# Kernel optimization log

Hardware: AMD Instinct MI355X
Metric: run time of the kernel (lower is better)

Reference implementation:

```python
import jax, jax.numpy as jnp
import numpy as np

D = 128
NH = 8
L = 3
DFF = 2048
DEPOT_IDX = 0
LN_EPS = 1e-5


def _ln(x, g, b):
    m = jnp.mean(x, -1, keepdims=True)
    v = jnp.mean((x - m) ** 2, -1, keepdims=True)
    return (x - m) / jnp.sqrt(v + LN_EPS) * g + b


def _mha(x, wqkv, bqkv, wo, bo):
    # torch nn.MultiheadAttention, batch_first, no dropout (eval)
    b, n, d = x.shape
    hd = d // NH
    qkv = x @ wqkv.T + bqkv                       # [b,n,3d]
    q, k, v = jnp.split(qkv, 3, axis=-1)
    sh = lambda t: t.reshape(b, n, NH, hd).transpose(0, 2, 1, 3)
    q, k, v = sh(q), sh(k), sh(v)
    att = jax.nn.softmax(jnp.einsum('bhqd,bhkd->bhqk', q, k) * (hd ** -0.5), axis=-1)
    o = jnp.einsum('bhqk,bhkd->bhqd', att, v).transpose(0, 2, 1, 3).reshape(b, n, d)
    return o @ wo.T + bo


def _encoder(c, w_inp, b_inp, wqkv, bqkv, wo, bo, w1, b1, w2, b2, g1, be1, g2, be2):
    h = c @ w_inp.T + b_inp                       # [b,n,d]

    def layer(h, p):
        (wqkv, bqkv, wo, bo, w1, b1, w2, b2, g1, be1, g2, be2) = p
        # post-LN TransformerEncoderLayer (torch default norm_first=False, relu)
        h = _ln(h + _mha(h, wqkv, bqkv, wo, bo), g1, be1)
        ff = jax.nn.relu(h @ w1.T + b1) @ w2.T + b2
        h = _ln(h + ff, g2, be2)
        return h, None

    h, _ = jax.lax.scan(layer, h, (wqkv, bqkv, wo, bo, w1, b1, w2, b2, g1, be1, g2, be2))
    return h


def _greedy(c, start_node, params):
    (w_inp, b_inp, wqkv, bqkv, wo, bo, w1, b1, w2, b2, g1, be1, g2, be2,
     wq, bq, wk, bk) = params
    b, n, _ = c.shape
    e = _encoder(c, w_inp, b_inp, wqkv, bqkv, wo, bo, w1, b1, w2, b2, g1, be1, g2, be2)
    kproj = e @ wk.T + bk                          # [b,n,d], hoisted (loop-invariant)
    scale = D ** (-0.5)
    neg = jnp.finfo(e.dtype).min
    bidx = jnp.arange(b)

    vis0 = jnp.zeros((b, n), bool).at[:, DEPOT_IDX].set(True)

    def step(carry, _):
        node, vis = carry
        mask = vis.at[bidx, node].set(True)
        q = e[bidx, node] @ wq.T + bq              # [b,d]
        logits = jnp.einsum('bd,bnd->bn', q, kproj) * scale
        logits = jnp.where(mask, neg, logits)
        nxt = jnp.argmax(logits, axis=-1)
        return (nxt, mask), (node, logits)

    (_, _), (tour, logits) = jax.lax.scan(step, (start_node, vis0), None, length=n - 1)
    return tour.T, logits.transpose(1, 0, 2)      # [b,n-1], [b,n-1,n]


def setup_inputs() -> dict:
    key = jax.random.key(0)
    ks = jax.random.split(key, 24)
    B, N = 512, 100
    w = lambda k, s: jax.random.normal(k, s, jnp.float32) * 0.05
    inp = {
        'c': jax.random.uniform(ks[0], (B, N, 2), jnp.float32),
        'start_node': jax.random.randint(ks[1], (B,), 1, N),
        'w_inp': w(ks[2], (D, 2)), 'b_inp': jnp.zeros((D,), jnp.float32),
        'wqkv': w(ks[3], (L, 3 * D, D)), 'bqkv': jnp.zeros((L, 3 * D), jnp.float32),
        'wo': w(ks[4], (L, D, D)), 'bo': jnp.zeros((L, D), jnp.float32),
        'w1': w(ks[5], (L, DFF, D)), 'b1': jnp.zeros((L, DFF), jnp.float32),
        'w2': w(ks[6], (L, D, DFF)), 'b2': jnp.zeros((L, D), jnp.float32),
        'g1': jnp.ones((L, D), jnp.float32), 'be1': jnp.zeros((L, D), jnp.float32),
        'g2': jnp.ones((L, D), jnp.float32), 'be2': jnp.zeros((L, D), jnp.float32),
        'wq': w(ks[7], (D, D)), 'bq': jnp.zeros((D,), jnp.float32),
        'wk': w(ks[8], (D, D)), 'bk': jnp.zeros((D,), jnp.float32),
    }
    return inp


def reference(c, start_node, w_inp, b_inp, wqkv, bqkv, wo, bo, w1, b1, w2, b2,
              g1, be1, g2, be2, wq, bq, wk, bk):
    params = (w_inp, b_inp, wqkv, bqkv, wo, bo, w1, b1, w2, b2,
              g1, be1, g2, be2, wq, bq, wk, bk)
    tour, logits = _greedy(c, start_node, params)
    return tour, logits
```

## Files before the change

### kernel.cpp

```cpp
#include <hip/hip_runtime.h>
#include <hip/hip_bf16.h>
#include <math.h>

#define D 128
#define NH 8
#define HD 16
#define NL 3
#define DFF 2048
#define NNODE 100
#define BATCH 512
#define M_TOT (BATCH * NNODE)
#define LN_EPS 1e-5f
#define NEGW (-3.0e+38f)

typedef __attribute__((ext_vector_type(8))) short bf16x8;
typedef __attribute__((ext_vector_type(4))) float f32x4;
typedef __attribute__((ext_vector_type(8))) unsigned short u16x8;

__device__ __forceinline__ unsigned short f2bf(float x) {
  unsigned u = __float_as_uint(x);
  u = u + 0x7FFFu + ((u >> 16) & 1u);
  return (unsigned short)(u >> 16);
}
__device__ __forceinline__ float bf2f(unsigned short s) {
  return __uint_as_float(((unsigned)s) << 16);
}

__global__ __launch_bounds__(256) void k_split(
    const float* __restrict__ src, unsigned short* __restrict__ hi,
    unsigned short* __restrict__ lo, int n) {
  int i = blockIdx.x * 256 + threadIdx.x;
  if (i >= n) return;
  float x = src[i];
  unsigned short h = f2bf(x);
  hi[i] = h;
  lo[i] = f2bf(x - bf2f(h));
}

__global__ __launch_bounds__(256) void k_inproj(
    const float* __restrict__ c, const float* __restrict__ w,
    const float* __restrict__ b, float* __restrict__ h,
    unsigned short* __restrict__ hhi, unsigned short* __restrict__ hlo) {
  int idx = blockIdx.x * 256 + threadIdx.x;
  if (idx >= M_TOT * D) return;
  int m = idx >> 7, d = idx & 127;
  float v = c[m * 2] * w[d * 2] + c[m * 2 + 1] * w[d * 2 + 1] + b[d];
  h[idx] = v;
  unsigned short t = f2bf(v);
  hhi[idx] = t;
  hlo[idx] = f2bf(v - bf2f(t));
}

__global__ __launch_bounds__(256) void k_gemm3(
    const unsigned short* __restrict__ Ah, const unsigned short* __restrict__ Al,
    const unsigned short* __restrict__ Wh, const unsigned short* __restrict__ Wl,
    const float* __restrict__ bias,
    float* __restrict__ C, unsigned short* __restrict__ Chi,
    unsigned short* __restrict__ Clo, int M, int N, int K, int relu_split) {
  __shared__ unsigned short sAh[64 * 40], sAl[64 * 40];
  __shared__ unsigned short sWh[128 * 40], sWl[128 * 40];
  const int m0 = blockIdx.x * 64, n0 = blockIdx.y * 128;
  const int tid = threadIdx.x, lane = tid & 63, wid = tid >> 6;
  const int wr = wid >> 1, wc = wid & 1;
  const int lr = lane & 15, lg = lane >> 4;
  f32x4 acc[2][4];
#pragma unroll
  for (int a = 0; a < 2; ++a)
#pragma unroll
    for (int b = 0; b < 4; ++b) acc[a][b] = (f32x4){0.f, 0.f, 0.f, 0.f};
  const int ar = tid >> 2, ak = (tid & 3) * 8;
  const int wrr = tid >> 1, wkk = (tid & 1) * 16;
  const bool a_ok = (m0 + ar) < M;
  const long long a_base = (long long)(m0 + ar) * K + ak;
  const long long w_base = (long long)(n0 + wrr) * K + wkk;
  for (int k0 = 0; k0 < K; k0 += 32) {
    u16x8 vah = {0, 0, 0, 0, 0, 0, 0, 0}, val = {0, 0, 0, 0, 0, 0, 0, 0};
    if (a_ok) {
      vah = *(const u16x8*)(Ah + a_base + k0);
      val = *(const u16x8*)(Al + a_base + k0);
    }
    u16x8 vwh0 = *(const u16x8*)(Wh + w_base + k0);
    u16x8 vwh1 = *(const u16x8*)(Wh + w_base + k0 + 8);
    u16x8 vwl0 = *(const u16x8*)(Wl + w_base + k0);
    u16x8 vwl1 = *(const u16x8*)(Wl + w_base + k0 + 8);
    __syncthreads();
    *(u16x8*)&sAh[ar * 40 + ak] = vah;
    *(u16x8*)&sAl[ar * 40 + ak] = val;
    *(u16x8*)&sWh[wrr * 40 + wkk] = vwh0;
    *(u16x8*)&sWh[wrr * 40 + wkk + 8] = vwh1;
    *(u16x8*)&sWl[wrr * 40 + wkk] = vwl0;
    *(u16x8*)&sWl[wrr * 40 + wkk + 8] = vwl1;
    __syncthreads();
    bf16x8 fah[2], fal[2], fwh[4], fwl[4];
#pragma unroll
    for (int fm = 0; fm < 2; ++fm) {
      int o = (wr * 32 + fm * 16 + lr) * 40 + lg * 8;
      fah[fm] = *(const bf16x8*)&sAh[o];
      fal[fm] = *(const bf16x8*)&sAl[o];
    }
#pragma unroll
    for (int fn = 0; fn < 4; ++fn) {
      int o = (wc * 64 + fn * 16 + lr) * 40 + lg * 8;
      fwh[fn] = *(const bf16x8*)&sWh[o];
      fwl[fn] = *(const bf16x8*)&sWl[o];
    }
#pragma unroll
    for (int fm = 0; fm < 2; ++fm)
#pragma unroll
      for (int fn = 0; fn < 4; ++fn) {
        acc[fm][fn] = __builtin_amdgcn_mfma_f32_16x16x32_bf16(
            fah[fm], fwl[fn], acc[fm][fn], 0, 0, 0);
        acc[fm][fn] = __builtin_amdgcn_mfma_f32_16x16x32_bf16(
            fal[fm], fwh[fn], acc[fm][fn], 0, 0, 0);
        acc[fm][fn] = __builtin_amdgcn_mfma_f32_16x16x32_bf16(
            fah[fm], fwh[fn], acc[fm][fn], 0, 0, 0);
      }
  }
#pragma unroll
  for (int fm = 0; fm < 2; ++fm) {
    int rb = m0 + wr * 32 + fm * 16 + lg * 4;
#pragma unroll
    for (int fn = 0; fn < 4; ++fn) {
      int col = n0 + wc * 64 + fn * 16 + lr;
      float bv = bias[col];
#pragma unroll
      for (int j = 0; j < 4; ++j) {
        int row = rb + j;
        if (row < M) {
          float v = acc[fm][fn][j] + bv;
          if (relu_split) {
            v = fmaxf(v, 0.f);
            unsigned short hv = f2bf(v);
            long long o = (long long)row * N + col;
            Chi[o] = hv;
            Clo[o] = f2bf(v - bf2f(hv));
          } else {
            C[(long long)row * N + col] = v;
          }
        }
      }
    }
  }
}

__global__ __launch_bounds__(256) void k_gemm3_ln(
    const unsigned short* __restrict__ Ah, const unsigned short* __restrict__ Al,
    const unsigned short* __restrict__ Wh, const unsigned short* __restrict__ Wl,
    const float* __restrict__ bias, const float* __restrict__ g,
    const float* __restrict__ be, float* __restrict__ hres,
    unsigned short* __restrict__ hhi, unsigned short* __restrict__ hlo,
    int M, int K) {
  __shared__ unsigned short sAh[64 * 40], sAl[64 * 40];
  __shared__ unsigned short sWh[128 * 40], sWl[128 * 40];
  __shared__ float redS[64][2];
  __shared__ float redQ[64][2];
  const int m0 = blockIdx.x * 64;
  const int tid = threadIdx.x, lane = tid & 63, wid = tid >> 6;
  const int wr = wid >> 1, wc = wid & 1;
  const int lr = lane & 15, lg = lane >> 4;
  f32x4 acc[2][4];
#pragma unroll
  for (int a = 0; a < 2; ++a)
#pragma unroll
    for (int b = 0; b < 4; ++b) acc[a][b] = (f32x4){0.f, 0.f, 0.f, 0.f};
  const int ar = tid >> 2, ak = (tid & 3) * 8;
  const int wrr = tid >> 1, wkk = (tid & 1) * 16;
  const bool a_ok = (m0 + ar) < M;
  const long long a_base = (long long)(m0 + ar) * K + ak;
  const long long w_base = (long long)wrr * K + wkk;
  for (int k0 = 0; k0 < K; k0 += 32) {
    u16x8 vah = {0, 0, 0, 0, 0, 0, 0, 0}, val = {0, 0, 0, 0, 0, 0, 0, 0};
    if (a_ok) {
      vah = *(const u16x8*)(Ah + a_base + k0);
      val = *(const u16x8*)(Al + a_base + k0);
    }
    u16x8 vwh0 = *(const u16x8*)(Wh + w_base + k0);
    u16x8 vwh1 = *(const u16x8*)(Wh + w_base + k0 + 8);
    u16x8 vwl0 = *(const u16x8*)(Wl + w_base + k0);
    u16x8 vwl1 = *(const u16x8*)(Wl + w_base + k0 + 8);
    __syncthreads();
    *(u16x8*)&sAh[ar * 40 + ak] = vah;
    *(u16x8*)&sAl[ar * 40 + ak] = val;
    *(u16x8*)&sWh[wrr * 40 + wkk] = vwh0;
    *(u16x8*)&sWh[wrr * 40 + wkk + 8] = vwh1;
    *(u16x8*)&sWl[wrr * 40 + wkk] = vwl0;
    *(u16x8*)&sWl[wrr * 40 + wkk + 8] = vwl1;
    __syncthreads();
    bf16x8 fah[2], fal[2], fwh[4], fwl[4];
#pragma unroll
    for (int fm = 0; fm < 2; ++fm) {
      int o = (wr * 32 + fm * 16 + lr) * 40 + lg * 8;
      fah[fm] = *(const bf16x8*)&sAh[o];
      fal[fm] = *(const bf16x8*)&sAl[o];
    }
#pragma unroll
    for (int fn = 0; fn < 4; ++fn) {
      int o = (wc * 64 + fn * 16 + lr) * 40 + lg * 8;
      fwh[fn] = *(const bf16x8*)&sWh[o];
      fwl[fn] = *(const bf16x8*)&sWl[o];
    }
#pragma unroll
    for (int fm = 0; fm < 2; ++fm)
#pragma unroll
      for (int fn = 0; fn < 4; ++fn) {
        acc[fm][fn] = __builtin_amdgcn_mfma_f32_16x16x32_bf16(
            fah[fm], fwl[fn], acc[fm][fn], 0, 0, 0);
        acc[fm][fn] = __builtin_amdgcn_mfma_f32_16x16x32_bf16(
            fal[fm], fwh[fn], acc[fm][fn], 0, 0, 0);
        acc[fm][fn] = __builtin_amdgcn_mfma_f32_16x16x32_bf16(
            fah[fm], fwh[fn], acc[fm][fn], 0, 0, 0);
      }
  }
  float x[2][4][4];
#pragma unroll
  for (int fm = 0; fm < 2; ++fm)
#pragma unroll
    for (int fn = 0; fn < 4; ++fn) {
      int col = wc * 64 + fn * 16 + lr;
      float bv = bias[col];
#pragma unroll
      for (int j = 0; j < 4; ++j) {
        int row = m0 + wr * 32 + fm * 16 + lg * 4 + j;
        float r = (row < M) ? hres[(long long)row * D + col] : 0.f;
        x[fm][fn][j] = acc[fm][fn][j] + bv + r;
      }
    }
#pragma unroll
  for (int fm = 0; fm < 2; ++fm)
#pragma unroll
    for (int j = 0; j < 4; ++j) {
      float s = x[fm][0][j] + x[fm][1][j] + x[fm][2][j] + x[fm][3][j];
      s += __shfl_xor(s, 1);
      s += __shfl_xor(s, 2);
      s += __shfl_xor(s, 4);
      s += __shfl_xor(s, 8);
      if (lr == 0) redS[wr * 32 + fm * 16 + lg * 4 + j][wc] = s;
    }
  __syncthreads();
  float mean[2][4];
#pragma unroll
  for (int fm = 0; fm < 2; ++fm)
#pragma unroll
    for (int j = 0; j < 4; ++j) {
      int rl = wr * 32 + fm * 16 + lg * 4 + j;
      mean[fm][j] = (redS[rl][0] + redS[rl][1]) * (1.f / 128.f);
      float d0 = x[fm][0][j] - mean[fm][j];
      float d1 = x[fm][1][j] - mean[fm][j];
      float d2 = x[fm][2][j] - mean[fm][j];
      float d3 = x[fm][3][j] - mean[fm][j];
      float q = d0 * d0 + d1 * d1 + d2 * d2 + d3 * d3;
      q += __shfl_xor(q, 1);
      q += __shfl_xor(q, 2);
      q += __shfl_xor(q, 4);
      q += __shfl_xor(q, 8);
      if (lr == 0) redQ[rl][wc] = q;
    }
  __syncthreads();
#pragma unroll
  for (int fm = 0; fm < 2; ++fm)
#pragma unroll
    for (int j = 0; j < 4; ++j) {
      int rl = wr * 32 + fm * 16 + lg * 4 + j;
      int row = m0 + rl;
      if (row >= M) continue;
      float var = (redQ[rl][0] + redQ[rl][1]) * (1.f / 128.f);
      float sd = sqrtf(var + LN_EPS);
#pragma unroll
      for (int fn = 0; fn < 4; ++fn) {
        int col = wc * 64 + fn * 16 + lr;
        float o = (x[fm][fn][j] - mean[fm][j]) / sd * g[col] + be[col];
        long long ix = (long long)row * D + col;
        hres[ix] = o;
        unsigned short t = f2bf(o);
        hhi[ix] = t;
        hlo[ix] = f2bf(o - bf2f(t));
      }
    }
}

__global__ __launch_bounds__(256) void k_gemm(
    const float* __restrict__ A, long long sA,
    const float* __restrict__ W, long long sW,
    const float* __restrict__ bias,
    float* __restrict__ C, long long sC,
    int M, int N, int K, float scale, int relu) {
  __shared__ float As[32][72];
  __shared__ float Ws[32][72];
  A += (long long)blockIdx.z * sA;
  W += (long long)blockIdx.z * sW;
  C += (long long)blockIdx.z * sC;
  int m0 = blockIdx.x * 64, n0 = blockIdx.y * 64;
  int tid = threadIdx.x;
  int lx = tid & 31, ly = tid >> 5;
  int tc = tid & 15, tr = tid >> 4;
  float acc[4][4] = {};
  for (int k0 = 0; k0 < K; k0 += 32) {
#pragma unroll
    for (int i = 0; i < 8; ++i) {
      int m = m0 + ly + i * 8;
      As[lx][ly + i * 8] = (m < M) ? A[(long long)m * K + k0 + lx] : 0.f;
      int n = n0 + ly + i * 8;
      Ws[lx][ly + i * 8] = (n < N) ? W[(long long)n * K + k0 + lx] : 0.f;
    }
    __syncthreads();
#pragma unroll
    for (int k = 0; k < 32; ++k) {
      float4 av = *(const float4*)&As[k][tr * 4];
      float4 wv = *(const float4*)&Ws[k][tc * 4];
      const float* ap = (const float*)&av;
      const float* wp = (const float*)&wv;
#pragma unroll
      for (int i = 0; i < 4; ++i)
#pragma unroll
        for (int j = 0; j < 4; ++j)
          acc[i][j] = fmaf(ap[i], wp[j], acc[i][j]);
    }
    __syncthreads();
  }
#pragma unroll
  for (int i = 0; i < 4; ++i) {
    int m = m0 + tr * 4 + i;
    if (m >= M) continue;
#pragma unroll
    for (int j = 0; j < 4; ++j) {
      int n = n0 + tc * 4 + j;
      if (n >= N) continue;
      float v = acc[i][j] * scale;
      if (bias) v += bias[n];
      if (relu) v = fmaxf(v, 0.f);
      C[(long long)m * N + n] = v;
    }
  }
}

__global__ __launch_bounds__(256) void k_attn(
    const float* __restrict__ qkv, unsigned short* __restrict__ aoh,
    unsigned short* __restrict__ aol) {
  __shared__ float Qs[NNODE][20];
  __shared__ float Ks[NNODE][20];
  __shared__ float Vs[NNODE][20];
  __shared__ float Ss[NNODE][101];
  int bh = blockIdx.x;
  int b = bh >> 3, hh = bh & 7;
  const float* base = qkv + (long long)b * NNODE * 384 + hh * HD;
  int tid = threadIdx.x;
  for (int idx = tid; idx < NNODE * HD; idx += 256) {
    int n = idx >> 4, d2 = idx & 15;
    Qs[n][d2] = base[(long long)n * 384 + d2];
    Ks[n][d2] = base[(long long)n * 384 + 128 + d2];
    Vs[n][d2] = base[(long long)n * 384 + 256 + d2];
  }
  __syncthreads();
  for (int p = tid; p < NNODE * NNODE; p += 256) {
    int i = p / 100, j = p - i * 100;
    const float4* qv = (const float4*)&Qs[i][0];
    const float4* kv = (const float4*)&Ks[j][0];
    float s = 0.f;
#pragma unroll
    for (int t = 0; t < 4; ++t) {
      float4 q = qv[t], k = kv[t];
      s = fmaf(q.x, k.x, s);
      s = fmaf(q.y, k.y, s);
      s = fmaf(q.z, k.z, s);
      s = fmaf(q.w, k.w, s);
    }
    Ss[i][j] = s * 0.25f;
  }
  __syncthreads();
  float* red = (float*)Qs;
  int r = tid >> 1, hf = tid & 1;
  float* row = &Ss[r][hf * 50];
  if (tid < 200) {
    float mx = row[0];
    for (int j = 1; j < 50; ++j) mx = fmaxf(mx, row[j]);
    red[tid] = mx;
  }
  __syncthreads();
  if (tid < 200) {
    float mx = fmaxf(red[r * 2], red[r * 2 + 1]);
    float sum = 0.f;
    for (int j = 0; j < 50; ++j) {
      float e = expf(row[j] - mx);
      row[j] = e;
      sum += e;
    }
    red[256 + tid] = sum;
  }
  __syncthreads();
  if (tid < 200) {
    float tot = red[256 + r * 2] + red[256 + r * 2 + 1];
    for (int j = 0; j < 50; ++j) row[j] = row[j] / tot;
  }
  __syncthreads();
  for (int p = tid; p < NNODE * HD; p += 256) {
    int i = p >> 4, d2 = p & 15;
    float o = 0.f;
    for (int k = 0; k < NNODE; ++k) o = fmaf(Ss[i][k], Vs[k][d2], o);
    long long idx = ((long long)b * NNODE + i) * D + hh * HD + d2;
    unsigned short hv = f2bf(o);
    aoh[idx] = hv;
    aol[idx] = f2bf(o - bf2f(hv));
  }
}

__global__ __launch_bounds__(64) void k_decode(
    const float* __restrict__ S, const int* __restrict__ start,
    float* __restrict__ tour, float* __restrict__ logits) {
  __shared__ float Sl[NNODE * NNODE];
  int b = blockIdx.x;
  const float* Sg = S + (long long)b * NNODE * NNODE;
  int l = threadIdx.x;
  for (int i = l; i < NNODE * NNODE; i += 64) Sl[i] = Sg[i];
  __syncthreads();
  unsigned long long visLo = 1ull, visHi = 0ull;
  int node = start[b];
  float* lg = logits + (long long)b * 99 * 100;
  for (int t = 0; t < 99; ++t) {
    if (node < 64) visLo |= 1ull << node;
    else visHi |= 1ull << (node - 64);
    const float* row = &Sl[node * 100];
    float c0 = ((visLo >> l) & 1ull) ? NEGW : row[l];
    float c1 = NEGW;
    int j2 = l + 64;
    if (j2 < NNODE && !((visHi >> l) & 1ull)) c1 = row[j2];
    lg[t * 100 + l] = c0;
    if (j2 < NNODE) lg[t * 100 + j2] = c1;
    if (l == 0) tour[b * 99 + t] = (float)node;
    float v = c0;
    int idx = l;
    if (c1 > v) { v = c1; idx = j2; }
    for (int off = 32; off; off >>= 1) {
      float ov = __shfl_xor(v, off);
      int oi = __shfl_xor(idx, off);
      if (ov > v || (ov == v && oi < idx)) { v = ov; idx = oi; }
    }
    node = idx;
  }
}

extern "C" void kernel_launch(void* const* d_in, const int* in_sizes, int n_in,
                              void* d_out, int out_size, void* d_ws, size_t ws_size,
                              hipStream_t stream) {
  const float* c     = (const float*)d_in[0];
  const int*   start = (const int*)d_in[1];
  const float* w_inp = (const float*)d_in[2];
  const float* b_inp = (const float*)d_in[3];
  const float* wqkv  = (const float*)d_in[4];
  const float* bqkv  = (const float*)d_in[5];
  const float* wo    = (const float*)d_in[6];
  const float* bo    = (const float*)d_in[7];
  const float* w1    = (const float*)d_in[8];
  const float* b1    = (const float*)d_in[9];
  const float* w2    = (const float*)d_in[10];
  const float* b2    = (const float*)d_in[11];
  const float* g1    = (const float*)d_in[12];
  const float* be1   = (const float*)d_in[13];
  const float* g2    = (const float*)d_in[14];
  const float* be2   = (const float*)d_in[15];
  const float* wq    = (const float*)d_in[16];
  const float* bq    = (const float*)d_in[17];
  const float* wk    = (const float*)d_in[18];
  const float* bk    = (const float*)d_in[19];

  float* h = (float*)d_ws;
  unsigned short* h_hi = (unsigned short*)((char*)d_ws + 26214400);
  unsigned short* h_lo = h_hi + (size_t)M_TOT * D;
  unsigned short* wsp  = (unsigned short*)((char*)d_ws + 52428800);
  unsigned short* wqkvh = wsp;
  unsigned short* wqkvl = wsp + 147456;
  unsigned short* woh   = wsp + 294912;
  unsigned short* wol   = wsp + 344064;
  unsigned short* w1h   = wsp + 393216;
  unsigned short* w1l   = wsp + 1179648;
  unsigned short* w2h   = wsp + 1966080;
  unsigned short* w2l   = wsp + 2752512;
  unsigned short* wqh   = wsp + 3538944;
  unsigned short* wql   = wsp + 3555328;
  unsigned short* wkh   = wsp + 3571712;
  unsigned short* wkl   = wsp + 3588096;
  float* wsArena = (float*)((char*)d_ws + 59637760);
  long long R = (long long)ws_size - 59637760LL;
  if (R < 0) R = 0;

  float* tour   = (float*)d_out;
  float* logits = (float*)d_out + (size_t)BATCH * (NNODE - 1);
  long long LBYTES = (long long)BATCH * (NNODE - 1) * NNODE * 4;

  float* encArena = (R >= LBYTES) ? wsArena : logits;
  long long E = (R >= LBYTES) ? R : LBYTES;

  long long CB = E / 204800;
  if (CB < 1) CB = 1;
  if (CB > BATCH) CB = BATCH;
  long long RB = (E / 8192) & ~3LL;
  if (RB < 4) RB = 4;
  if (RB > M_TOT) RB = M_TOT;
  long long CB2 = R / 142400;
  if (CB2 < 1) CB2 = 1;
  if (CB2 > BATCH) CB2 = BATCH;

  k_split<<<576, 256, 0, stream>>>(wqkv, wqkvh, wqkvl, 147456);
  k_split<<<192, 256, 0, stream>>>(wo, woh, wol, 49152);
  k_split<<<3072, 256, 0, stream>>>(w1, w1h, w1l, 786432);
  k_split<<<3072, 256, 0, stream>>>(w2, w2h, w2l, 786432);
  k_split<<<64, 256, 0, stream>>>(wq, wqh, wql, 16384);
  k_split<<<64, 256, 0, stream>>>(wk, wkh, wkl, 16384);

  k_inproj<<<(M_TOT * D + 255) / 256, 256, 0, stream>>>(c, w_inp, b_inp, h,
                                                        h_hi, h_lo);

  for (int l = 0; l < NL; ++l) {
    unsigned short* wqkvh_l = wqkvh + (size_t)l * 49152;
    unsigned short* wqkvl_l = wqkvl + (size_t)l * 49152;
    unsigned short* woh_l = woh + (size_t)l * 16384;
    unsigned short* wol_l = wol + (size_t)l * 16384;
    unsigned short* w1h_l = w1h + (size_t)l * 262144;
    unsigned short* w1l_l = w1l + (size_t)l * 262144;
    unsigned short* w2h_l = w2h + (size_t)l * 262144;
    unsigned short* w2l_l = w2l + (size_t)l * 262144;
    const float* bqkv_l = bqkv + (size_t)l * 384;
    const float* bo_l = bo + (size_t)l * D;
    const float* b1_l = b1 + (size_t)l * DFF;
    const float* b2_l = b2 + (size_t)l * D;
    const float* g1_l = g1 + (size_t)l * D;
    const float* be1_l = be1 + (size_t)l * D;
    const float* g2_l = g2 + (size_t)l * D;
    const float* be2_l = be2 + (size_t)l * D;

    for (long long b0 = 0; b0 < BATCH; b0 += CB) {
      long long cb = (BATCH - b0 < CB) ? (BATCH - b0) : CB;
      long long rows = cb * NNODE;
      float* qkvbuf = encArena;
      unsigned short* aoh = (unsigned short*)(qkvbuf + rows * 384);
      unsigned short* aol = aoh + rows * D;
      float* hrow = h + b0 * NNODE * D;
      unsigned short* hhir = h_hi + b0 * NNODE * D;
      unsigned short* hlor = h_lo + b0 * NNODE * D;
      k_gemm3<<<dim3((unsigned)((rows + 63) / 64), 3), 256, 0, stream>>>(
          hhir, hlor, wqkvh_l, wqkvl_l, bqkv_l, qkvbuf, nullptr, nullptr,
          (int)rows, 384, D, 0);
      k_attn<<<(unsigned)(cb * NH), 256, 0, stream>>>(qkvbuf, aoh, aol);
      k_gemm3_ln<<<(unsigned)((rows + 63) / 64), 256, 0, stream>>>(
          aoh, aol, woh_l, wol_l, bo_l, g1_l, be1_l, hrow, hhir, hlor,
          (int)rows, D);
    }

    for (long long r0 = 0; r0 < M_TOT; r0 += RB) {
      long long mr = (M_TOT - r0 < RB) ? (M_TOT - r0) : RB;
      unsigned short* ff1h = (unsigned short*)encArena;
      unsigned short* ff1l = ff1h + mr * DFF;
      float* hrow = h + r0 * D;
      unsigned short* hhir = h_hi + r0 * D;
      unsigned short* hlor = h_lo + r0 * D;
      k_gemm3<<<dim3((unsigned)((mr + 63) / 64), DFF / 128), 256, 0, stream>>>(
          hhir, hlor, w1h_l, w1l_l, b1_l, nullptr, ff1h, ff1l,
          (int)mr, DFF, D, 1);
      k_gemm3_ln<<<(unsigned)((mr + 63) / 64), 256, 0, stream>>>(
          ff1h, ff1l, w2h_l, w2l_l, b2_l, g2_l, be2_l, hrow, hhir, hlor,
          (int)mr, DFF);
    }
  }

  for (long long b0 = 0; b0 < BATCH; b0 += CB2) {
    long long cb = (BATCH - b0 < CB2) ? (BATCH - b0) : CB2;
    long long rows = cb * NNODE;
    float* qp = wsArena;
    float* kp = qp + rows * D;
    float* Sb = kp + rows * D;
    unsigned short* hhir = h_hi + b0 * NNODE * D;
    unsigned short* hlor = h_lo + b0 * NNODE * D;
    k_gemm3<<<dim3((unsigned)((rows + 63) / 64), 1), 256, 0, stream>>>(
        hhir, hlor, wqh, wql, bq, qp, nullptr, nullptr, (int)rows, D, D, 0);
    k_gemm3<<<dim3((unsigned)((rows + 63) / 64), 1), 256, 0, stream>>>(
        hhir, hlor, wkh, wkl, bk, kp, nullptr, nullptr, (int)rows, D, D, 0);
    k_gemm<<<dim3(2, 2, (unsigned)cb), 256, 0, stream>>>(
        qp, (long long)NNODE * D, kp, (long long)NNODE * D, nullptr,
        Sb, (long long)NNODE * NNODE, NNODE, NNODE, D,
        0.08838834764831845f, 0);
    k_decode<<<(unsigned)cb, 64, 0, stream>>>(Sb, start + b0, tour + b0 * 99,
                                              logits + b0 * 99 * 100);
  }
}
```

Baseline: 2.279 ms.

## Load GEMM fragments directly from global memory and retune attention kernel

Both split-bf16 GEMM kernels stop staging A and W tiles through shared memory. Each lane now loads its MFMA fragments straight from global memory, which removes the LDS traffic and two barriers per k-step. In exchange every wave reloads the same operands from global/L2 with strided access, and out-of-range rows are clamped rather than zeroed. The attention kernel moves to 512 threads, rotates the K layout in shared memory to cut bank conflicts, and has each thread compute four output dims with float4 V reads.

Result: slower. 3.524 ms (+54.7%).

```diff
diff --git a/kernel.cpp b/kernel.cpp
--- a/kernel.cpp
+++ b/kernel.cpp
@@ -15,7 +15,6 @@
 
 typedef __attribute__((ext_vector_type(8))) short bf16x8;
 typedef __attribute__((ext_vector_type(4))) float f32x4;
-typedef __attribute__((ext_vector_type(8))) unsigned short u16x8;
 
 __device__ __forceinline__ unsigned short f2bf(float x) {
   unsigned u = __float_as_uint(x);
@@ -57,8 +56,6 @@
     const float* __restrict__ bias,
     float* __restrict__ C, unsigned short* __restrict__ Chi,
     unsigned short* __restrict__ Clo, int M, int N, int K, int relu_split) {
-  __shared__ unsigned short sAh[64 * 40], sAl[64 * 40];
-  __shared__ unsigned short sWh[128 * 40], sWl[128 * 40];
   const int m0 = blockIdx.x * 64, n0 = blockIdx.y * 128;
   const int tid = threadIdx.x, lane = tid & 63, wid = tid >> 6;
   const int wr = wid >> 1, wc = wid & 1;
@@ -68,41 +65,28 @@
   for (int a = 0; a < 2; ++a)
 #pragma unroll
     for (int b = 0; b < 4; ++b) acc[a][b] = (f32x4){0.f, 0.f, 0.f, 0.f};
-  const int ar = tid >> 2, ak = (tid & 3) * 8;
-  const int wrr = tid >> 1, wkk = (tid & 1) * 16;
-  const bool a_ok = (m0 + ar) < M;
-  const long long a_base = (long long)(m0 + ar) * K + ak;
-  const long long w_base = (long long)(n0 + wrr) * K + wkk;
+  long long arow[2], wrow[4];
+#pragma unroll
+  for (int fm = 0; fm < 2; ++fm) {
+    int r = m0 + wr * 32 + fm * 16 + lr;
+    if (r > M - 1) r = M - 1;
+    arow[fm] = (long long)r * K + lg * 8;
+  }
+#pragma unroll
+  for (int fn = 0; fn < 4; ++fn)
+    wrow[fn] = (long long)(n0 + wc * 64 + fn * 16 + lr) * K + lg * 8;
+#pragma unroll 2
   for (int k0 = 0; k0 < K; k0 += 32) {
-    u16x8 vah = {0, 0, 0, 0, 0, 0, 0, 0}, val = {0, 0, 0, 0, 0, 0, 0, 0};
-    if (a_ok) {
-      vah = *(const u16x8*)(Ah + a_base + k0);
-      val = *(const u16x8*)(Al + a_base + k0);
-    }
-    u16x8 vwh0 = *(const u16x8*)(Wh + w_base + k0);
-    u16x8 vwh1 = *(const u16x8*)(Wh + w_base + k0 + 8);
-    u16x8 vwl0 = *(const u16x8*)(Wl + w_base + k0);
-    u16x8 vwl1 = *(const u16x8*)(Wl + w_base + k0 + 8);
-    __syncthreads();
-    *(u16x8*)&sAh[ar * 40 + ak] = vah;
-    *(u16x8*)&sAl[ar * 40 + ak] = val;
-    *(u16x8*)&sWh[wrr * 40 + wkk] = vwh0;
-    *(u16x8*)&sWh[wrr * 40 + wkk + 8] = vwh1;
-    *(u16x8*)&sWl[wrr * 40 + wkk] = vwl0;
-    *(u16x8*)&sWl[wrr * 40 + wkk + 8] = vwl1;
-    __syncthreads();
     bf16x8 fah[2], fal[2], fwh[4], fwl[4];
 #pragma unroll
     for (int fm = 0; fm < 2; ++fm) {
-      int o = (wr * 32 + fm * 16 + lr) * 40 + lg * 8;
-      fah[fm] = *(const bf16x8*)&sAh[o];
-      fal[fm] = *(const bf16x8*)&sAl[o];
+      fah[fm] = *(const bf16x8*)(Ah + arow[fm] + k0);
+      fal[fm] = *(const bf16x8*)(Al + arow[fm] + k0);
     }
 #pragma unroll
     for (int fn = 0; fn < 4; ++fn) {
-      int o = (wc * 64 + fn * 16 + lr) * 40 + lg * 8;
-      fwh[fn] = *(const bf16x8*)&sWh[o];
-      fwl[fn] = *(const bf16x8*)&sWl[o];
+      fwh[fn] = *(const bf16x8*)(Wh + wrow[fn] + k0);
+      fwl[fn] = *(const bf16x8*)(Wl + wrow[fn] + k0);
     }
 #pragma unroll
     for (int fm = 0; fm < 2; ++fm)
@@ -150,8 +134,6 @@
     const float* __restrict__ be, float* __restrict__ hres,
     unsigned short* __restrict__ hhi, unsigned short* __restrict__ hlo,
     int M, int K) {
-  __shared__ unsigned short sAh[64 * 40], sAl[64 * 40];
-  __shared__ unsigned short sWh[128 * 40], sWl[128 * 40];
   __shared__ float redS[64][2];
   __shared__ float redQ[64][2];
   const int m0 = blockIdx.x * 64;
@@ -163,41 +145,28 @@
   for (int a = 0; a < 2; ++a)
 #pragma unroll
     for (int b = 0; b < 4; ++b) acc[a][b] = (f32x4){0.f, 0.f, 0.f, 0.f};
-  const int ar = tid >> 2, ak = (tid & 3) * 8;
-  const int wrr = tid >> 1, wkk = (tid & 1) * 16;
-  const bool a_ok = (m0 + ar) < M;
-  const long long a_base = (long long)(m0 + ar) * K + ak;
-  const long long w_base = (long long)wrr * K + wkk;
+  long long arow[2], wrow[4];
+#pragma unroll
+  for (int fm = 0; fm < 2; ++fm) {
+    int r = m0 + wr * 32 + fm * 16 + lr;
+    if (r > M - 1) r = M - 1;
+    arow[fm] = (long long)r * K + lg * 8;
+  }
+#pragma unroll
+  for (int fn = 0; fn < 4; ++fn)
+    wrow[fn] = (long long)(wc * 64 + fn * 16 + lr) * K + lg * 8;
+#pragma unroll 2
   for (int k0 = 0; k0 < K; k0 += 32) {
-    u16x8 vah = {0, 0, 0, 0, 0, 0, 0, 0}, val = {0, 0, 0, 0, 0, 0, 0, 0};
-    if (a_ok) {
-      vah = *(const u16x8*)(Ah + a_base + k0);
-      val = *(const u16x8*)(Al + a_base + k0);
-    }
-    u16x8 vwh0 = *(const u16x8*)(Wh + w_base + k0);
-    u16x8 vwh1 = *(const u16x8*)(Wh + w_base + k0 + 8);
-    u16x8 vwl0 = *(const u16x8*)(Wl + w_base + k0);
-    u16x8 vwl1 = *(const u16x8*)(Wl + w_base + k0 + 8);
-    __syncthreads();
-    *(u16x8*)&sAh[ar * 40 + ak] = vah;
-    *(u16x8*)&sAl[ar * 40 + ak] = val;
-    *(u16x8*)&sWh[wrr * 40 + wkk] = vwh0;
-    *(u16x8*)&sWh[wrr * 40 + wkk + 8] = vwh1;
-    *(u16x8*)&sWl[wrr * 40 + wkk] = vwl0;
-    *(u16x8*)&sWl[wrr * 40 + wkk + 8] = vwl1;
-    __syncthreads();
     bf16x8 fah[2], fal[2], fwh[4], fwl[4];
 #pragma unroll
     for (int fm = 0; fm < 2; ++fm) {
-      int o = (wr * 32 + fm * 16 + lr) * 40 + lg * 8;
-      fah[fm] = *(const bf16x8*)&sAh[o];
-      fal[fm] = *(const bf16x8*)&sAl[o];
+      fah[fm] = *(const bf16x8*)(Ah + arow[fm] + k0);
+      fal[fm] = *(const bf16x8*)(Al + arow[fm] + k0);
     }
 #pragma unroll
     for (int fn = 0; fn < 4; ++fn) {
-      int o = (wc * 64 + fn * 16 + lr) * 40 + lg * 8;
-      fwh[fn] = *(const bf16x8*)&sWh[o];
-      fwl[fn] = *(const bf16x8*)&sWl[o];
+      fwh[fn] = *(const bf16x8*)(Wh + wrow[fn] + k0);
+      fwl[fn] = *(const bf16x8*)(Wl + wrow[fn] + k0);
     }
 #pragma unroll
     for (int fm = 0; fm < 2; ++fm)
@@ -333,7 +302,7 @@
   }
 }
 
-__global__ __launch_bounds__(256) void k_attn(
+__global__ __launch_bounds__(512) void k_attn(
     const float* __restrict__ qkv, unsigned short* __restrict__ aoh,
     unsigned short* __restrict__ aol) {
   __shared__ float Qs[NNODE][20];
@@ -344,21 +313,26 @@
   int b = bh >> 3, hh = bh & 7;
   const float* base = qkv + (long long)b * NNODE * 384 + hh * HD;
   int tid = threadIdx.x;
-  for (int idx = tid; idx < NNODE * HD; idx += 256) {
+  for (int idx = tid; idx < NNODE * HD; idx += 512) {
     int n = idx >> 4, d2 = idx & 15;
-    Qs[n][d2] = base[(long long)n * 384 + d2];
-    Ks[n][d2] = base[(long long)n * 384 + 128 + d2];
-    Vs[n][d2] = base[(long long)n * 384 + 256 + d2];
-  }
-  __syncthreads();
-  for (int p = tid; p < NNODE * NNODE; p += 256) {
+    float qv = base[(long long)n * 384 + d2];
+    float kv = base[(long long)n * 384 + 128 + d2];
+    float vv = base[(long long)n * 384 + 256 + d2];
+    Qs[n][d2] = qv;
+    int kp = ((((d2 >> 2) + (n >> 3)) & 3) << 2) | (d2 & 3);
+    Ks[n][kp] = kv;
+    Vs[n][d2] = vv;
+  }
+  __syncthreads();
+  for (int p = tid; p < NNODE * NNODE; p += 512) {
     int i = p / 100, j = p - i * 100;
+    int rot = (j >> 3) & 3;
     const float4* qv = (const float4*)&Qs[i][0];
-    const float4* kv = (const float4*)&Ks[j][0];
     float s = 0.f;
 #pragma unroll
     for (int t = 0; t < 4; ++t) {
-      float4 q = qv[t], k = kv[t];
+      float4 q = qv[t];
+      float4 k = *(const float4*)&Ks[j][(((t + rot) & 3) << 2)];
       s = fmaf(q.x, k.x, s);
       s = fmaf(q.y, k.y, s);
       s = fmaf(q.z, k.z, s);
@@ -392,14 +366,25 @@
     for (int j = 0; j < 50; ++j) row[j] = row[j] / tot;
   }
   __syncthreads();
-  for (int p = tid; p < NNODE * HD; p += 256) {
-    int i = p >> 4, d2 = p & 15;
-    float o = 0.f;
-    for (int k = 0; k < NNODE; ++k) o = fmaf(Ss[i][k], Vs[k][d2], o);
-    long long idx = ((long long)b * NNODE + i) * D + hh * HD + d2;
-    unsigned short hv = f2bf(o);
-    aoh[idx] = hv;
-    aol[idx] = f2bf(o - bf2f(hv));
+  for (int p = tid; p < NNODE * 4; p += 512) {
+    int i = p >> 2, q = p & 3;
+    float4 o = {0.f, 0.f, 0.f, 0.f};
+    for (int k = 0; k < NNODE; ++k) {
+      float sv = Ss[i][k];
+      float4 v = *(const float4*)&Vs[k][q << 2];
+      o.x = fmaf(sv, v.x, o.x);
+      o.y = fmaf(sv, v.y, o.y);
+      o.z = fmaf(sv, v.z, o.z);
+      o.w = fmaf(sv, v.w, o.w);
+    }
+    long long idx = ((long long)b * NNODE + i) * D + hh * HD + (q << 2);
+    const float* op = (const float*)&o;
+#pragma unroll
+    for (int e = 0; e < 4; ++e) {
+      unsigned short hv = f2bf(op[e]);
+      aoh[idx + e] = hv;
+      aol[idx + e] = f2bf(op[e] - bf2f(hv));
+    }
   }
 }
 
@@ -539,7 +524,7 @@
       k_gemm3<<<dim3((unsigned)((rows + 63) / 64), 3), 256, 0, stream>>>(
           hhir, hlor, wqkvh_l, wqkvl_l, bqkv_l, qkvbuf, nullptr, nullptr,
           (int)rows, 384, D, 0);
-      k_attn<<<(unsigned)(cb * NH), 256, 0, stream>>>(qkvbuf, aoh, aol);
+      k_attn<<<(unsigned)(cb * NH), 512, 0, stream>>>(qkvbuf, aoh, aol);
       k_gemm3_ln<<<(unsigned)((rows + 63) / 64), 256, 0, stream>>>(
           aoh, aol, woh_l, wol_l, bo_l, g1_l, be1_l, hrow, hhir, hlor,
           (int)rows, D);
```
